# Performance work log

Hardware: AMD Instinct MI355X
Metric: run time of the kernel (lower is better)

The kernel has to match this reference:

```python
import jax, jax.numpy as jnp
import numpy as np

IP = 10  # power-iteration steps


def setup_inputs() -> dict:
    key = jax.random.key(0)
    k1, k2 = jax.random.split(key)
    B, C, H, W = 16, 512, 64, 64
    x = jax.random.normal(k1, (B, C, H, W), dtype=jnp.float32)
    # random start vector for power iteration (torch: FloatTensor.normal_(0,1))
    v = jax.random.normal(k2, (B, C, 1), dtype=jnp.float32)
    return {"x": x, "v": v}


def reference(x, v):
    B, C, H, W = x.shape
    # w = x.view(B,C,HW).permute(0,2,1) -> (B, HW, C)
    w = jnp.transpose(x.reshape(B, C, H * W), (0, 2, 1))
    # W_s = w^T w : (B, C, C)
    Ws = jnp.einsum('bnc,bnd->bcd', w, w)

    def step(vc, _):
        vc = jnp.matmul(Ws, vc)                                   # (B,C,1)
        vc = vc / jnp.linalg.norm(vc, axis=(1, 2), keepdims=True)  # per-batch L2 norm
        return vc, None

    v, _ = jax.lax.scan(step, v, None, length=IP)
    # u = W v, normalized : (B, HW, 1)
    u = jnp.matmul(w, v)
    u = u / jnp.linalg.norm(u, axis=(1, 2), keepdims=True)
    # z = u v^T : (B, HW, C) -> (B, C, H, W)
    z = jnp.matmul(u, jnp.transpose(v, (0, 2, 1)))
    z = jnp.transpose(z, (0, 2, 1)).reshape(B, C, H, W)
    return x + z
```

## Files before the change

kernel.cpp:

```cpp
#include <hip/hip_runtime.h>
#include <stdint.h>

#define NB 16
#define NC 512
#define NHW 4096

typedef unsigned short u16;
typedef __bf16 bf16x8 __attribute__((ext_vector_type(8)));
typedef float f32x4 __attribute__((ext_vector_type(4)));
typedef unsigned short u16x8 __attribute__((ext_vector_type(8)));
typedef unsigned short u16x4 __attribute__((ext_vector_type(4)));

#define AS1 __attribute__((address_space(1)))
#define AS3 __attribute__((address_space(3)))

__device__ __forceinline__ float bf2f(u16 h) {
    union { unsigned u; float f; } a; a.u = ((unsigned)h) << 16; return a.f;
}
__device__ __forceinline__ u16 f2bf(float f) {
    union { float f; unsigned u; } a; a.f = f;
    unsigned u = a.u;
    return (u16)((u + 0x7FFFu + ((u >> 16) & 1u)) >> 16);
}

__global__ __launch_bounds__(256) void k_to_bf16(const float* __restrict__ x,
                                                 u16* __restrict__ xb) {
    int i = blockIdx.x * 256 + threadIdx.x;
    f32x4 v = ((const f32x4*)x)[i];
    u16x4 o;
    o[0] = f2bf(v[0]); o[1] = f2bf(v[1]); o[2] = f2bf(v[2]); o[3] = f2bf(v[3]);
    ((u16x4*)xb)[i] = o;
}

__global__ __launch_bounds__(256, 2)
void k_gemm_bt(const u16* __restrict__ Ab, const u16* __restrict__ Bb,
               u16* __restrict__ Cb, int K, int N,
               size_t sA, size_t sB, size_t sC, float scale) {
    __shared__ u16 As[2][64 * 32];
    __shared__ u16 Bs[2][128 * 32];
    const int tid = threadIdx.x;
    const int wave = tid >> 6, lane = tid & 63;
    const int b = blockIdx.z;
    const u16* A  = Ab + (size_t)b * sA + (size_t)blockIdx.x * 64 * K;
    const u16* Bm = Bb + (size_t)b * sB + (size_t)blockIdx.y * 128 * K;

    const int srow = tid >> 2;
    const int scol = (tid & 3) * 8;
    const u16* ag0 = A  + (size_t)srow * K + scol;
    const u16* bg0 = Bm + (size_t)srow * K + scol;
    const u16* bg1 = bg0 + (size_t)64 * K;

#define STAGE(BUF, KO)                                                         \
    {                                                                          \
        __builtin_amdgcn_global_load_lds((AS1 void*)(ag0 + (KO)),              \
            (AS3 void*)(&As[BUF][wave * 512]), 16, 0, 0);                      \
        __builtin_amdgcn_global_load_lds((AS1 void*)(bg0 + (KO)),              \
            (AS3 void*)(&Bs[BUF][wave * 512]), 16, 0, 0);                      \
        __builtin_amdgcn_global_load_lds((AS1 void*)(bg1 + (KO)),              \
            (AS3 void*)(&Bs[BUF][2048 + wave * 512]), 16, 0, 0);               \
    }

    f32x4 acc[4][2];
#pragma unroll
    for (int i = 0; i < 4; i++)
#pragma unroll
        for (int j = 0; j < 2; j++) acc[i][j] = f32x4{0.f, 0.f, 0.f, 0.f};

    const int cn = wave * 32;
    const int m16 = lane & 15, quad = lane >> 4;

#define COMPUTE(BUF)                                                           \
    {                                                                          \
        bf16x8 af[4], bfr[2];                                                  \
        _Pragma("unroll")                                                      \
        for (int mi = 0; mi < 4; mi++)                                         \
            af[mi] = *(const bf16x8*)&As[BUF][(mi * 16 + m16) * 32 +           \
                                             quad * 8];                        \
        _Pragma("unroll")                                                      \
        for (int ni = 0; ni < 2; ni++)                                         \
            bfr[ni] = *(const bf16x8*)&Bs[BUF][(cn + ni * 16 + m16) * 32 +     \
                                              quad * 8];                       \
        _Pragma("unroll")                                                      \
        for (int mi = 0; mi < 4; mi++)                                         \
            _Pragma("unroll")                                                  \
            for (int ni = 0; ni < 2; ni++)                                     \
                acc[mi][ni] = __builtin_amdgcn_mfma_f32_16x16x32_bf16(         \
                    af[mi], bfr[ni], acc[mi][ni], 0, 0, 0);                    \
    }

    STAGE(0, 0);
    __syncthreads();

    for (int k0 = 0; k0 < K; k0 += 64) {
        STAGE(1, k0 + 32);
        COMPUTE(0);
        __syncthreads();
        if (k0 + 64 < K) STAGE(0, k0 + 64);
        COMPUTE(1);
        __syncthreads();
    }

    u16* Co = Cb + (size_t)b * sC + ((size_t)blockIdx.x * 64) * N +
              (size_t)blockIdx.y * 128;
    const int rq = quad * 4;
#pragma unroll
    for (int mi = 0; mi < 4; mi++)
#pragma unroll
        for (int ni = 0; ni < 2; ni++)
#pragma unroll
            for (int r = 0; r < 4; r++) {
                int row = mi * 16 + rq + r;
                int col = cn + ni * 16 + m16;
                Co[(size_t)row * N + col] = f2bf(acc[mi][ni][r] * scale);
            }
#undef STAGE
#undef COMPUTE
}

__global__ __launch_bounds__(1024, 1)
void k_power_iter(const u16* __restrict__ S2, const float* __restrict__ v0,
                  float* __restrict__ vhat) {
    const int b = blockIdx.x, tid = threadIdx.x;
    __shared__ float va[NC], vb[NC];
    __shared__ float part[NC][16];
    __shared__ float red[16];
    const u16* Mb = S2 + (size_t)b * NC * NC;
    const int cg = tid & 15;
    const int r0 = tid >> 4;
    if (tid < NC) va[tid] = v0[b * NC + tid];
    float* cur = va;
    float* nxt = vb;
    __syncthreads();

    for (int it = 0; it < 5; ++it) {
        float c[4][8];
#pragma unroll
        for (int p = 0; p < 4; p++) {
            f32x4 lo = *(const f32x4*)&cur[cg * 8 + p * 128];
            f32x4 hi = *(const f32x4*)&cur[cg * 8 + p * 128 + 4];
            c[p][0] = lo[0]; c[p][1] = lo[1]; c[p][2] = lo[2]; c[p][3] = lo[3];
            c[p][4] = hi[0]; c[p][5] = hi[1]; c[p][6] = hi[2]; c[p][7] = hi[3];
        }
#pragma unroll 2
        for (int pass = 0; pass < 8; ++pass) {
            const int r = pass * 64 + r0;
            const u16* row = Mb + (size_t)r * NC + cg * 8;
            u16x8 m[4];
#pragma unroll
            for (int p = 0; p < 4; p++) m[p] = *(const u16x8*)(row + p * 128);
            float a0 = 0.f, a1 = 0.f, a2 = 0.f, a3 = 0.f;
#pragma unroll
            for (int j = 0; j < 8; j++) {
                a0 += bf2f(m[0][j]) * c[0][j];
                a1 += bf2f(m[1][j]) * c[1][j];
                a2 += bf2f(m[2][j]) * c[2][j];
                a3 += bf2f(m[3][j]) * c[3][j];
            }
            part[r][cg] = (a0 + a1) + (a2 + a3);
        }
        __syncthreads();
        if (tid < NC) {
            f32x4 s0 = *(const f32x4*)&part[tid][0];
            f32x4 s1 = *(const f32x4*)&part[tid][4];
            f32x4 s2 = *(const f32x4*)&part[tid][8];
            f32x4 s3 = *(const f32x4*)&part[tid][12];
            f32x4 s = (s0 + s1) + (s2 + s3);
            nxt[tid] = (s[0] + s[1]) + (s[2] + s[3]);
        }
        __syncthreads();
        float* t = cur; cur = nxt; nxt = t;
    }

    float mv = (tid < NC) ? cur[tid] : 0.f;
    float x = mv * mv;
#pragma unroll
    for (int o = 32; o > 0; o >>= 1) x += __shfl_down(x, o, 64);
    if ((tid & 63) == 0) red[tid >> 6] = x;
    __syncthreads();
    float n = red[0];
#pragma unroll
    for (int w = 1; w < 16; w++) n += red[w];
    if (tid < NC) vhat[b * NC + tid] = mv * rsqrtf(n);
}

__global__ __launch_bounds__(256)
void k_compute_t(const u16* __restrict__ xb, const float* __restrict__ vhat,
                 float* __restrict__ tp) {
    const int b = blockIdx.z, cc = blockIdx.y, nc = blockIdx.x, tid = threadIdx.x;
    __shared__ float vsh[128];
    if (tid < 128) vsh[tid] = vhat[b * NC + cc * 128 + tid];
    __syncthreads();
    const int n0 = nc * 2048 + tid * 8;
    const u16* xp = xb + (size_t)b * NC * NHW + (size_t)cc * 128 * NHW + n0;
    float acc[8] = {0.f, 0.f, 0.f, 0.f, 0.f, 0.f, 0.f, 0.f};
    for (int c = 0; c < 128; c++) {
        u16x8 w = *(const u16x8*)xp;
        xp += NHW;
        float vc = vsh[c];
#pragma unroll
        for (int j = 0; j < 8; j++) acc[j] += bf2f(w[j]) * vc;
    }
    float* dst = tp + (size_t)(b * 4 + cc) * NHW + n0;
    *(f32x4*)dst       = f32x4{acc[0], acc[1], acc[2], acc[3]};
    *(f32x4*)(dst + 4) = f32x4{acc[4], acc[5], acc[6], acc[7]};
}

__global__ __launch_bounds__(1024, 1)
void k_tnorm(const float* __restrict__ tp, float* __restrict__ tsum,
             float* __restrict__ sinv) {
    const int b = blockIdx.x, tid = threadIdx.x;
    __shared__ float red[16];
    const int n0 = tid * 4;
    f32x4 s = f32x4{0.f, 0.f, 0.f, 0.f};
#pragma unroll
    for (int p = 0; p < 4; p++)
        s += *(const f32x4*)(tp + (size_t)(b * 4 + p) * NHW + n0);
    *(f32x4*)(tsum + (size_t)b * NHW + n0) = s;
    float ss = s[0] * s[0] + s[1] * s[1] + s[2] * s[2] + s[3] * s[3];
#pragma unroll
    for (int o = 32; o > 0; o >>= 1) ss += __shfl_down(ss, o, 64);
    if ((tid & 63) == 0) red[tid >> 6] = ss;
    __syncthreads();
    if (tid == 0) {
        float n = red[0];
#pragma unroll
        for (int w = 1; w < 16; w++) n += red[w];
        sinv[b] = rsqrtf(n);
    }
}

__global__ __launch_bounds__(256)
void k_epilogue(const float* __restrict__ x, const float* __restrict__ tsum,
                const float* __restrict__ vhat, const float* __restrict__ sinv,
                float* __restrict__ out) {
    const int b = blockIdx.z, cc = blockIdx.y, nc = blockIdx.x, tid = threadIdx.x;
    __shared__ float tl[1024];
    __shared__ float cf[64];
    const int nbase = nc * 1024, cbase = cc * 64;
    const float si = sinv[b];
    for (int i = tid; i < 1024; i += 256)
        tl[i] = tsum[(size_t)b * NHW + nbase + i];
    if (tid < 64) cf[tid] = vhat[b * NC + cbase + tid] * si;
    __syncthreads();
    f32x4 tv = ((const f32x4*)tl)[tid];
    for (int rr = 0; rr < 64; rr++) {
        size_t off = ((size_t)(b * NC + cbase + rr)) * NHW + nbase + tid * 4;
        f32x4 xv = *(const f32x4*)(x + off);
        float c = cf[rr];
        f32x4 o = xv + tv * c;
        *(f32x4*)(out + off) = o;
    }
}

extern "C" void kernel_launch(void* const* d_in, const int* in_sizes, int n_in,
                              void* d_out, int out_size, void* d_ws, size_t ws_size,
                              hipStream_t stream) {
    const float* x  = (const float*)d_in[0];
    const float* v0 = (const float*)d_in[1];
    float* out = (float*)d_out;

    char* ws = (char*)d_ws;
    u16* xb     = (u16*)ws;
    u16* S      = (u16*)(ws + 67108864);
    u16* S2     = (u16*)(ws + 67108864 + 8388608);
    float* vhat = (float*)(ws + 83886080);
    float* tp   = (float*)(ws + 83886080 + 65536);
    float* tsum = (float*)(ws + 83886080 + 65536 + 1048576);
    float* sinv = (float*)(ws + 83886080 + 65536 + 1048576 + 262144);

    k_to_bf16<<<dim3(32768), dim3(256), 0, stream>>>(x, xb);
    k_gemm_bt<<<dim3(8, 4, NB), dim3(256), 0, stream>>>(
        xb, xb, S, NHW, NC, (size_t)NC * NHW, (size_t)NC * NHW, (size_t)NC * NC,
        1.f / 4096.f);
    k_gemm_bt<<<dim3(8, 4, NB), dim3(256), 0, stream>>>(
        S, S, S2, NC, NC, (size_t)NC * NC, (size_t)NC * NC, (size_t)NC * NC,
        1.f);
    k_power_iter<<<dim3(NB), dim3(1024), 0, stream>>>(S2, v0, vhat);
    k_compute_t<<<dim3(2, 4, NB), dim3(256), 0, stream>>>(xb, vhat, tp);
    k_tnorm<<<dim3(NB), dim3(1024), 0, stream>>>(tp, tsum, sinv);
    k_epilogue<<<dim3(4, 8, NB), dim3(256), 0, stream>>>(x, tsum, vhat, sinv, out);
}
```

Baseline: 410.8 us.

## Enlarge GEMM tile to 128x128 with 4-stage LDS pipeline and swizzle

Rewrites the batched Gram GEMM to use 128x128 output tiles with a 2x2 wave layout, a four-buffer global_load_lds prefetch ring driven by explicit vmcnt waits and raw barriers, and an XOR swizzle on the K-column offset to reduce LDS bank conflicts. The aim is more MFMA work per loaded byte and deeper overlap of memory latency with compute. In exchange, the grid shrinks from 512 to 256 blocks, occupancy drops to one block per SIMD group, and LDS use grows. The loop also assumes K is a multiple of 128 and at least 256.

After: 395.0 us. -3.8%, faster.

```diff
diff --git a/kernel.cpp b/kernel.cpp
--- a/kernel.cpp
+++ b/kernel.cpp
@@ -32,21 +32,22 @@
     ((u16x4*)xb)[i] = o;
 }
 
-__global__ __launch_bounds__(256, 2)
+__global__ __launch_bounds__(256, 1)
 void k_gemm_bt(const u16* __restrict__ Ab, const u16* __restrict__ Bb,
                u16* __restrict__ Cb, int K, int N,
                size_t sA, size_t sB, size_t sC, float scale) {
-    __shared__ u16 As[2][64 * 32];
-    __shared__ u16 Bs[2][128 * 32];
+    __shared__ u16 As[4][128 * 32];
+    __shared__ u16 Bs[4][128 * 32];
     const int tid = threadIdx.x;
     const int wave = tid >> 6, lane = tid & 63;
     const int b = blockIdx.z;
-    const u16* A  = Ab + (size_t)b * sA + (size_t)blockIdx.x * 64 * K;
+    const u16* A  = Ab + (size_t)b * sA + (size_t)blockIdx.x * 128 * K;
     const u16* Bm = Bb + (size_t)b * sB + (size_t)blockIdx.y * 128 * K;
 
     const int srow = tid >> 2;
-    const int scol = (tid & 3) * 8;
+    const int scol = ((tid & 3) ^ ((srow >> 1) & 3)) * 8;
     const u16* ag0 = A  + (size_t)srow * K + scol;
+    const u16* ag1 = ag0 + (size_t)64 * K;
     const u16* bg0 = Bm + (size_t)srow * K + scol;
     const u16* bg1 = bg0 + (size_t)64 * K;
 
@@ -54,67 +55,98 @@
     {                                                                          \
         __builtin_amdgcn_global_load_lds((AS1 void*)(ag0 + (KO)),              \
             (AS3 void*)(&As[BUF][wave * 512]), 16, 0, 0);                      \
+        __builtin_amdgcn_global_load_lds((AS1 void*)(ag1 + (KO)),              \
+            (AS3 void*)(&As[BUF][2048 + wave * 512]), 16, 0, 0);               \
         __builtin_amdgcn_global_load_lds((AS1 void*)(bg0 + (KO)),              \
             (AS3 void*)(&Bs[BUF][wave * 512]), 16, 0, 0);                      \
         __builtin_amdgcn_global_load_lds((AS1 void*)(bg1 + (KO)),              \
             (AS3 void*)(&Bs[BUF][2048 + wave * 512]), 16, 0, 0);               \
     }
 
-    f32x4 acc[4][2];
+    f32x4 acc[4][4];
 #pragma unroll
     for (int i = 0; i < 4; i++)
 #pragma unroll
-        for (int j = 0; j < 2; j++) acc[i][j] = f32x4{0.f, 0.f, 0.f, 0.f};
-
-    const int cn = wave * 32;
+        for (int j = 0; j < 4; j++) acc[i][j] = f32x4{0.f, 0.f, 0.f, 0.f};
+
+    const int rm = (wave & 1) * 64;
+    const int rn = (wave >> 1) * 64;
     const int m16 = lane & 15, quad = lane >> 4;
+    const int qsw8 = (quad ^ ((m16 >> 1) & 3)) * 8;
 
 #define COMPUTE(BUF)                                                           \
     {                                                                          \
-        bf16x8 af[4], bfr[2];                                                  \
+        bf16x8 af[4], bfr[4];                                                  \
         _Pragma("unroll")                                                      \
         for (int mi = 0; mi < 4; mi++)                                         \
-            af[mi] = *(const bf16x8*)&As[BUF][(mi * 16 + m16) * 32 +           \
-                                             quad * 8];                        \
+            af[mi] = *(const bf16x8*)&As[BUF][(rm + mi * 16 + m16) * 32 +      \
+                                             qsw8];                            \
         _Pragma("unroll")                                                      \
-        for (int ni = 0; ni < 2; ni++)                                         \
-            bfr[ni] = *(const bf16x8*)&Bs[BUF][(cn + ni * 16 + m16) * 32 +     \
-                                              quad * 8];                       \
+        for (int ni = 0; ni < 4; ni++)                                         \
+            bfr[ni] = *(const bf16x8*)&Bs[BUF][(rn + ni * 16 + m16) * 32 +     \
+                                              qsw8];                           \
         _Pragma("unroll")                                                      \
         for (int mi = 0; mi < 4; mi++)                                         \
             _Pragma("unroll")                                                  \
-            for (int ni = 0; ni < 2; ni++)                                     \
+            for (int ni = 0; ni < 4; ni++)                                     \
                 acc[mi][ni] = __builtin_amdgcn_mfma_f32_16x16x32_bf16(         \
                     af[mi], bfr[ni], acc[mi][ni], 0, 0, 0);                    \
     }
 
+#define PHASE(J, KNEXT)                                                        \
+    asm volatile("s_waitcnt vmcnt(12)" ::: "memory");                          \
+    __builtin_amdgcn_s_barrier();                                              \
+    __builtin_amdgcn_sched_barrier(0);                                         \
+    COMPUTE(J);                                                                \
+    __builtin_amdgcn_sched_barrier(0);                                         \
+    __builtin_amdgcn_s_barrier();                                              \
+    STAGE(J, KNEXT);
+
     STAGE(0, 0);
-    __syncthreads();
-
-    for (int k0 = 0; k0 < K; k0 += 64) {
-        STAGE(1, k0 + 32);
-        COMPUTE(0);
-        __syncthreads();
-        if (k0 + 64 < K) STAGE(0, k0 + 64);
-        COMPUTE(1);
-        __syncthreads();
-    }
-
-    u16* Co = Cb + (size_t)b * sC + ((size_t)blockIdx.x * 64) * N +
+    STAGE(1, 32);
+    STAGE(2, 64);
+    STAGE(3, 96);
+
+    for (int kg = 0; kg + 256 <= K; kg += 128) {
+        PHASE(0, kg + 128);
+        PHASE(1, kg + 160);
+        PHASE(2, kg + 192);
+        PHASE(3, kg + 224);
+    }
+
+    asm volatile("s_waitcnt vmcnt(12)" ::: "memory");
+    __builtin_amdgcn_s_barrier();
+    __builtin_amdgcn_sched_barrier(0);
+    COMPUTE(0);
+    asm volatile("s_waitcnt vmcnt(8)" ::: "memory");
+    __builtin_amdgcn_s_barrier();
+    __builtin_amdgcn_sched_barrier(0);
+    COMPUTE(1);
+    asm volatile("s_waitcnt vmcnt(4)" ::: "memory");
+    __builtin_amdgcn_s_barrier();
+    __builtin_amdgcn_sched_barrier(0);
+    COMPUTE(2);
+    asm volatile("s_waitcnt vmcnt(0)" ::: "memory");
+    __builtin_amdgcn_s_barrier();
+    __builtin_amdgcn_sched_barrier(0);
+    COMPUTE(3);
+
+    u16* Co = Cb + (size_t)b * sC + ((size_t)blockIdx.x * 128) * N +
               (size_t)blockIdx.y * 128;
     const int rq = quad * 4;
 #pragma unroll
     for (int mi = 0; mi < 4; mi++)
 #pragma unroll
-        for (int ni = 0; ni < 2; ni++)
+        for (int ni = 0; ni < 4; ni++)
 #pragma unroll
             for (int r = 0; r < 4; r++) {
-                int row = mi * 16 + rq + r;
-                int col = cn + ni * 16 + m16;
+                int row = rm + mi * 16 + rq + r;
+                int col = rn + ni * 16 + m16;
                 Co[(size_t)row * N + col] = f2bf(acc[mi][ni][r] * scale);
             }
 #undef STAGE
 #undef COMPUTE
+#undef PHASE
 }
 
 __global__ __launch_bounds__(1024, 1)
@@ -269,10 +301,10 @@
     float* sinv = (float*)(ws + 83886080 + 65536 + 1048576 + 262144);
 
     k_to_bf16<<<dim3(32768), dim3(256), 0, stream>>>(x, xb);
-    k_gemm_bt<<<dim3(8, 4, NB), dim3(256), 0, stream>>>(
+    k_gemm_bt<<<dim3(4, 4, NB), dim3(256), 0, stream>>>(
         xb, xb, S, NHW, NC, (size_t)NC * NHW, (size_t)NC * NHW, (size_t)NC * NC,
         1.f / 4096.f);
-    k_gemm_bt<<<dim3(8, 4, NB), dim3(256), 0, stream>>>(
+    k_gemm_bt<<<dim3(4, 4, NB), dim3(256), 0, stream>>>(
         S, S, S2, NC, NC, (size_t)NC * NC, (size_t)NC * NC, (size_t)NC * NC,
         1.f);
     k_power_iter<<<dim3(NB), dim3(1024), 0, stream>>>(S2, v0, vhat);
```
